# Kernel optimization log

Measured on AMD Instinct MI355X. Metric: run time of the kernel, lower is better.

## Reference

```python
import jax, jax.numpy as jnp
import numpy as np

D_IN = 1024
D_OUT = 1024
N_HEADS = 16
HEAD_DIM = D_OUT // N_HEADS


def setup_inputs() -> dict:
    key = jax.random.key(0)
    ks = jax.random.split(key, 6)
    s = 0.02
    return {
        "x": jax.random.normal(ks[0], (2, 2048, D_IN), dtype=jnp.float32),
        "W_q": jax.random.normal(ks[1], (D_IN, D_OUT), dtype=jnp.float32) * s,
        "W_k": jax.random.normal(ks[2], (D_IN, D_OUT), dtype=jnp.float32) * s,
        "W_v": jax.random.normal(ks[3], (D_IN, D_OUT), dtype=jnp.float32) * s,
        "W_o": jax.random.normal(ks[4], (D_OUT, D_OUT), dtype=jnp.float32) * s,
        "b_o": jax.random.normal(ks[5], (D_OUT,), dtype=jnp.float32) * s,
    }


def reference(x, W_q, W_k, W_v, W_o, b_o):
    B, S, _ = x.shape
    # projections -> [B, H, S, Dh]
    def split_heads(t):
        return t.reshape(B, S, N_HEADS, HEAD_DIM).transpose(0, 2, 1, 3)
    q = split_heads(x @ W_q)
    k = split_heads(x @ W_k)
    v = split_heads(x @ W_v)
    scores = jnp.einsum("bhqd,bhkd->bhqk", q, k)
    causal = jnp.triu(jnp.ones((S, S), dtype=bool), k=1)  # True above diagonal
    scores = jnp.where(causal, -jnp.inf, scores)
    attn = jax.nn.softmax(scores / jnp.sqrt(jnp.float32(HEAD_DIM)), axis=-1)
    ctx = jnp.einsum("bhqk,bhkd->bhqd", attn, v)  # [B,H,S,Dh]
    ctx = ctx.transpose(0, 2, 1, 3).reshape(B, S, D_OUT)
    return ctx @ W_o + b_o
```

## Files before the change

kernel.cpp:

```cpp
#include <hip/hip_runtime.h>
#include <math.h>

typedef unsigned short u16;
typedef unsigned int u32;
typedef short v8s __attribute__((ext_vector_type(8)));
typedef float v4f __attribute__((ext_vector_type(4)));
typedef u16 u16x4v __attribute__((ext_vector_type(4)));
typedef u16 u16x8v __attribute__((ext_vector_type(8)));
typedef u32 u32x2 __attribute__((ext_vector_type(2)));

#define S_LEN 2048
#define D_MODEL 1024
#define DH 64
#define BS_ROWS 4096

#define QSCALE 0.1803368801111204f

#if __has_builtin(__builtin_amdgcn_exp2f)
#define EXP2(x) __builtin_amdgcn_exp2f(x)
#else
#define EXP2(x) __expf(0.6931471805599453f * (x))
#endif

__device__ __forceinline__ u16 f2bf(float f) {
    union { float f; unsigned int u; } c; c.f = f;
    unsigned int u = c.u;
    unsigned int r = (u + 0x7FFFu + ((u >> 16) & 1u)) >> 16;
    return (u16)r;
}
__device__ __forceinline__ u32 pack2bf(float a, float b) {
    u32 ua = __float_as_uint(a) + 0x8000u;
    u32 ub = __float_as_uint(b) + 0x8000u;
    return (ua >> 16) | (ub & 0xFFFF0000u);
}

__device__ __forceinline__ v4f mfma16(v8s a, v8s b, v4f c) {
    return __builtin_amdgcn_mfma_f32_16x16x32_bf16(a, b, c, 0, 0, 0);
}

__device__ __forceinline__ void gl_lds(const u16* g, u16* l) {
    __builtin_amdgcn_global_load_lds(
        (const __attribute__((address_space(1))) void*)g,
        (__attribute__((address_space(3))) void*)l, 16, 0, 0);
}

__global__ __launch_bounds__(256) void prep_kernel(const float* __restrict__ x,
                                                   const float* __restrict__ Wq,
                                                   const float* __restrict__ Wk,
                                                   const float* __restrict__ Wv,
                                                   const float* __restrict__ Wo,
                                                   u16* __restrict__ xb,
                                                   u16* __restrict__ wqkv,
                                                   u16* __restrict__ wo_t) {
    __shared__ u16 tile[64][72];
    int blk = blockIdx.x;
    int t = threadIdx.x;
    if (blk < 4096) {
        int i = blk * 256 + t;
        float4 v = ((const float4*)x)[i];
        u16x4v o;
        o[0] = f2bf(v.x); o[1] = f2bf(v.y); o[2] = f2bf(v.z); o[3] = f2bf(v.w);
        ((u16x4v*)xb)[i] = o;
        return;
    }
    int pb = blk - 4096;
    int z = pb >> 8;
    pb &= 255;
    const float* w = (z == 0) ? Wq : (z == 1) ? Wk : (z == 2) ? Wv : Wo;
    u16* wt = (z < 3) ? (wqkv + (size_t)z * 1024 * 1024) : wo_t;
    int k0 = (pb & 15) * 64, n0 = (pb >> 4) * 64;
    int tr = t >> 4;
    int tc = (t & 15) * 4;
#pragma unroll
    for (int i = 0; i < 4; ++i) {
        int k = tr + 16 * i;
        float4 v = *(const float4*)(w + (size_t)(k0 + k) * 1024 + n0 + tc);
        tile[tc + 0][k] = f2bf(v.x);
        tile[tc + 1][k] = f2bf(v.y);
        tile[tc + 2][k] = f2bf(v.z);
        tile[tc + 3][k] = f2bf(v.w);
    }
    __syncthreads();
#pragma unroll
    for (int i = 0; i < 4; ++i) {
        int n = tr + 16 * i;
        u16x4v o;
        o[0] = tile[n][tc]; o[1] = tile[n][tc + 1];
        o[2] = tile[n][tc + 2]; o[3] = tile[n][tc + 3];
        *(u16x4v*)(wt + (size_t)(n0 + n) * 1024 + k0 + tc) = o;
    }
}

template <int MODE>
__global__ __launch_bounds__(256, 3) void gemm_kernel(
    const u16* __restrict__ A, const u16* __restrict__ Bt,
    const float* __restrict__ bias,
    u16* __restrict__ q_out, u16* __restrict__ k_out, u16* __restrict__ v_out,
    float* __restrict__ out_f32) {
    constexpr int BN = (MODE == 0) ? 128 : 64;
    constexpr int MT = (MODE == 0) ? 4 : 2;
    constexpr int K = 1024;
    __shared__ __align__(16) u16 Smem[128 * 64 + BN * 64];
    u16* As = Smem;
    u16* Bs = Smem + 128 * 64;
    int tid = threadIdx.x;
    int lane = tid & 63;
    int w = tid >> 6;
    int n16 = lane & 15, quad = lane >> 4;
    int lrow = lane >> 3, lchunk = lane & 7;
    int m0 = blockIdx.y * 128, n0 = blockIdx.x * BN;
    int wm_off = (MODE == 0) ? (w >> 1) * 64 : w * 32;
    int wn_off = (MODE == 0) ? (w & 1) * 64 : 0;

    v4f acc[MT][4];
#pragma unroll
    for (int i = 0; i < MT; ++i)
#pragma unroll
        for (int j = 0; j < 4; ++j) acc[i][j] = v4f{0, 0, 0, 0};

    for (int k0 = 0; k0 < K; k0 += 64) {
#pragma unroll
        for (int i = 0; i < 4; ++i) {
            int r = w * 32 + i * 8 + lrow;
            int gc = lchunk ^ (r & 7);
            gl_lds(A + (size_t)(m0 + r) * K + k0 + gc * 8, As + (w * 32 + i * 8) * 64);
        }
        if (MODE == 0) {
#pragma unroll
            for (int i = 0; i < 4; ++i) {
                int r = w * 32 + i * 8 + lrow;
                int gc = lchunk ^ (r & 7);
                gl_lds(Bt + (size_t)(n0 + r) * K + k0 + gc * 8, Bs + (w * 32 + i * 8) * 64);
            }
        } else {
#pragma unroll
            for (int i = 0; i < 2; ++i) {
                int r = w * 16 + i * 8 + lrow;
                int gc = lchunk ^ (r & 7);
                gl_lds(Bt + (size_t)(n0 + r) * K + k0 + gc * 8, Bs + (w * 16 + i * 8) * 64);
            }
        }
        __syncthreads();
#pragma unroll
        for (int kk = 0; kk < 64; kk += 32) {
            v8s af[MT], bf[4];
#pragma unroll
            for (int mt = 0; mt < MT; ++mt) {
                int ra = wm_off + mt * 16 + n16;
                af[mt] = *(const v8s*)(As + ra * 64 + ((((kk >> 3) + quad) ^ (ra & 7)) << 3));
            }
#pragma unroll
            for (int nt = 0; nt < 4; ++nt) {
                int rb = wn_off + nt * 16 + n16;
                bf[nt] = *(const v8s*)(Bs + rb * 64 + ((((kk >> 3) + quad) ^ (rb & 7)) << 3));
            }
#pragma unroll
            for (int mt = 0; mt < MT; ++mt)
#pragma unroll
                for (int nt = 0; nt < 4; ++nt)
                    acc[mt][nt] = mfma16(af[mt], bf[nt], acc[mt][nt]);
        }
        __syncthreads();
    }

    if (MODE == 1) {
#pragma unroll
        for (int mt = 0; mt < MT; ++mt)
#pragma unroll
            for (int nt = 0; nt < 4; ++nt)
#pragma unroll
                for (int r = 0; r < 4; ++r) {
                    int row = m0 + wm_off + mt * 16 + quad * 4 + r;
                    int col = n0 + nt * 16 + n16;
                    out_f32[(size_t)row * 1024 + col] = acc[mt][nt][r] + bias[col];
                }
        return;
    }

    int which = n0 >> 10;
    if (which < 2) {
        u16* dst = which ? k_out : q_out;
        float sc = which ? 1.0f : QSCALE;
#pragma unroll
        for (int mt = 0; mt < 4; ++mt)
#pragma unroll
            for (int nt = 0; nt < 4; ++nt) {
                int colb = n0 + wn_off + nt * 16;
                int rowb = m0 + wm_off + mt * 16 + quad * 4;
                int hb = (colb & 1023) >> 6;
                int d = (colb & 63) + n16;
                int b = rowb >> 11, s = rowb & 2047;
                int bh = b * 16 + hb;
#pragma unroll
                for (int r = 0; r < 4; ++r)
                    dst[((size_t)bh * S_LEN + s + r) * DH + d] = f2bf(acc[mt][nt][r] * sc);
            }
    } else {
        int b = m0 >> 11, s0 = m0 & 2047;
        u16* T = Smem;
#pragma unroll
        for (int p = 0; p < 2; ++p) {
            __syncthreads();
            if ((w & 1) == p) {
#pragma unroll
                for (int mt = 0; mt < 4; ++mt)
#pragma unroll
                    for (int nt = 0; nt < 4; ++nt) {
                        int d = nt * 16 + n16;
                        int sl = (w >> 1) * 64 + mt * 16 + quad * 4;
                        u16x4v pk;
#pragma unroll
                        for (int r = 0; r < 4; ++r) pk[r] = f2bf(acc[mt][nt][r]);
                        *(u16x4v*)(T + d * 136 + sl) = pk;
                    }
            }
            __syncthreads();
            int h = 2 * (blockIdx.x - 16) + p;
            int bh = b * 16 + h;
            int d = tid >> 2;
            int part = tid & 3;
            u16* gp = v_out + ((size_t)bh * DH + d) * S_LEN + s0 + part * 32;
            const u16* tp = T + d * 136 + part * 32;
#pragma unroll
            for (int i = 0; i < 4; ++i)
                *(u16x8v*)(gp + i * 8) = *(const u16x8v*)(tp + i * 8);
        }
    }
}

template <bool DIAG>
__device__ __forceinline__ void attn_step(const u16* __restrict__ ks,
                                          const u16* __restrict__ vs,
                                          u16* __restrict__ pw,
                                          v8s qa0, v8s qa1,
                                          v4f* acc, float& l,
                                          int n16, int quad, int wq) {
    v4f st[4];
#pragma unroll
    for (int nt = 0; nt < 4; ++nt) {
        int rk = nt * 16 + n16;
        const u16* kr = ks + rk * 64;
        v4f t = v4f{0, 0, 0, 0};
        t = mfma16(*(const v8s*)(kr + ((quad ^ (rk & 7)) << 3)), qa0, t);
        t = mfma16(*(const v8s*)(kr + (((4 + quad) ^ (rk & 7)) << 3)), qa1, t);
        st[nt] = t;
    }
    int h = n16 & 7;
    u16* prow = pw + n16 * 64;
#pragma unroll
    for (int nt = 0; nt < 4; ++nt) {
        float e[4];
#pragma unroll
        for (int r = 0; r < 4; ++r) {
            float v = EXP2(st[nt][r]);
            if (DIAG) {
                if (nt * 16 + quad * 4 + r > wq) v = 0.0f;
            }
            e[r] = v;
            l += v;
        }
        u32x2 pk;
        pk[0] = pack2bf(e[0], e[1]);
        pk[1] = pack2bf(e[2], e[3]);
        *(u32x2*)(prow + (((2 * nt + (quad >> 1)) ^ h) << 3) + (quad & 1) * 4) = pk;
    }
    v8s pa0 = *(const v8s*)(prow + ((quad ^ h) << 3));
    v8s pa1 = *(const v8s*)(prow + (((4 + quad) ^ h) << 3));
#pragma unroll
    for (int f = 0; f < 4; ++f) {
        int rv = f * 16 + n16;
        const u16* vr = vs + rv * 64;
        acc[f] = mfma16(pa0, *(const v8s*)(vr + ((quad ^ (rv & 7)) << 3)), acc[f]);
        acc[f] = mfma16(pa1, *(const v8s*)(vr + (((4 + quad) ^ (rv & 7)) << 3)), acc[f]);
    }
}

__global__ __launch_bounds__(256, 4) void attn_kernel(const u16* __restrict__ Qg,
                                                      const u16* __restrict__ Kg,
                                                      const u16* __restrict__ Vtg,
                                                      u16* __restrict__ ctx) {
    __shared__ __align__(16) u16 Ks[2][64 * 64];
    __shared__ __align__(16) u16 Vs[2][64 * 64];
    __shared__ __align__(16) u16 Ps[4][16 * 64];

    int i = blockIdx.x;
    int xcd = i & 7;
    int j = i >> 3;
    int bh = xcd * 4 + (j & 3);
    int idx = j >> 2;
    int i0 = idx & 7, m = idx >> 3;
    int qt = (m == 0) ? (31 - i0) : (m == 1) ? (16 + i0) : (m == 2) ? (15 - i0) : i0;
    int qbase = qt * 64;
    int tid = threadIdx.x;
    int w = tid >> 6;
    int lane = tid & 63;
    int n16 = lane & 15;
    int quad = lane >> 4;
    int lrow = lane >> 3, lchunk = lane & 7;

    const u16* Qb = Qg + (size_t)bh * (S_LEN * DH);
    const u16* Kb = Kg + (size_t)bh * (S_LEN * DH);
    const u16* Vtb = Vtg + (size_t)bh * (S_LEN * DH);
    u16* pw = Ps[w];
    int b = bh >> 4, h = bh & 15;
    int cur = 0;

    auto stage = [&](int kb, int buf) {
#pragma unroll
        for (int i2 = 0; i2 < 2; ++i2) {
            int r = w * 16 + i2 * 8 + lrow;
            int gc = lchunk ^ (r & 7);
            gl_lds(Kb + (size_t)(kb + r) * DH + gc * 8, &Ks[buf][(w * 16 + i2 * 8) * 64]);
            gl_lds(Vtb + (size_t)r * S_LEN + kb + gc * 8, &Vs[buf][(w * 16 + i2 * 8) * 64]);
        }
    };

    int qrow = qbase + w * 16 + n16;
    v8s qa0 = *(const v8s*)(Qb + (size_t)qrow * DH + quad * 8);
    v8s qa1 = *(const v8s*)(Qb + (size_t)qrow * DH + 32 + quad * 8);

    v4f acc[4];
#pragma unroll
    for (int f = 0; f < 4; ++f) acc[f] = v4f{0, 0, 0, 0};
    float l = 0.0f;
    int wq = w * 16 + n16;
    int nkb = qt + 1;

    stage(0, cur);
    for (int it = 0; it < nkb - 1; ++it) {
        __syncthreads();
        stage((it + 1) * 64, cur ^ 1);
        attn_step<false>(Ks[cur], Vs[cur], pw, qa0, qa1, acc, l, n16, quad, wq);
        cur ^= 1;
    }
    __syncthreads();
    attn_step<true>(Ks[cur], Vs[cur], pw, qa0, qa1, acc, l, n16, quad, wq);

    l += __shfl_xor(l, 16);
    l += __shfl_xor(l, 32);
#pragma unroll
    for (int r = 0; r < 4; ++r) {
        float lq = __shfl(l, quad * 4 + r);
        float inv = 1.0f / lq;
        int srow = qbase + w * 16 + quad * 4 + r;
        size_t base = ((size_t)(b * S_LEN + srow)) * D_MODEL + h * DH;
#pragma unroll
        for (int f = 0; f < 4; ++f)
            ctx[base + f * 16 + n16] = f2bf(acc[f][r] * inv);
    }
}

extern "C" void kernel_launch(void* const* d_in, const int* in_sizes, int n_in,
                              void* d_out, int out_size, void* d_ws, size_t ws_size,
                              hipStream_t stream) {
    const float* x  = (const float*)d_in[0];
    const float* Wq = (const float*)d_in[1];
    const float* Wk = (const float*)d_in[2];
    const float* Wv = (const float*)d_in[3];
    const float* Wo = (const float*)d_in[4];
    const float* bo = (const float*)d_in[5];
    float* out = (float*)d_out;

    char* ws = (char*)d_ws;
    u16* x_bf = (u16*)ws;   ws += (size_t)BS_ROWS * D_MODEL * 2;
    u16* wqkv = (u16*)ws;   ws += (size_t)3 * D_MODEL * D_MODEL * 2;
    u16* wo_t = (u16*)ws;   ws += (size_t)D_MODEL * D_MODEL * 2;
    u16* qbuf = (u16*)ws;   ws += (size_t)BS_ROWS * D_MODEL * 2;
    u16* kbuf = (u16*)ws;   ws += (size_t)BS_ROWS * D_MODEL * 2;
    u16* vtbuf = (u16*)ws;  ws += (size_t)BS_ROWS * D_MODEL * 2;
    u16* ctx = (u16*)ws;    ws += (size_t)BS_ROWS * D_MODEL * 2;

    prep_kernel<<<5120, 256, 0, stream>>>(x, Wq, Wk, Wv, Wo, x_bf, wqkv, wo_t);

    gemm_kernel<0><<<dim3(24, 32), 256, 0, stream>>>(x_bf, wqkv, nullptr,
                                                     qbuf, kbuf, vtbuf, nullptr);
    attn_kernel<<<1024, 256, 0, stream>>>(qbuf, kbuf, vtbuf, ctx);
    gemm_kernel<1><<<dim3(16, 32), 256, 0, stream>>>(ctx, wo_t, bo,
                                                     nullptr, nullptr, nullptr, out);
}
```

Before: 165.0 us.

## Process two 64-row query tiles per attention block to reuse staged K/V

```diff
diff --git a/kernel.cpp b/kernel.cpp
--- a/kernel.cpp
+++ b/kernel.cpp
@@ -275,7 +275,7 @@
     }
 }
 
-__global__ __launch_bounds__(256, 4) void attn_kernel(const u16* __restrict__ Qg,
+__global__ __launch_bounds__(256, 2) void attn_kernel(const u16* __restrict__ Qg,
                                                       const u16* __restrict__ Kg,
                                                       const u16* __restrict__ Vtg,
                                                       u16* __restrict__ ctx) {
@@ -283,14 +283,16 @@
     __shared__ __align__(16) u16 Vs[2][64 * 64];
     __shared__ __align__(16) u16 Ps[4][16 * 64];
 
-    int i = blockIdx.x;
-    int xcd = i & 7;
-    int j = i >> 3;
-    int bh = xcd * 4 + (j & 3);
-    int idx = j >> 2;
-    int i0 = idx & 7, m = idx >> 3;
-    int qt = (m == 0) ? (31 - i0) : (m == 1) ? (16 + i0) : (m == 2) ? (15 - i0) : i0;
-    int qbase = qt * 64;
+    int jj = blockIdx.x;
+    int xcd = jj & 7;
+    int jp = jj >> 3;
+    int t = jp & 3, u = jp >> 2;
+    int bh = xcd * 4 + t;
+    int us = (u + 4) & 15;
+    int b0 = (u < 8) ? u : 23 - u;
+    int b0s = (us < 8) ? us : 23 - us;
+    int qt = (t == 0) ? b0 : (t == 1) ? 15 - b0 : (t == 2) ? b0s : 15 - b0s;
+    int qbase = qt * 128;
     int tid = threadIdx.x;
     int w = tid >> 6;
     int lane = tid & 63;
@@ -310,43 +312,58 @@
         for (int i2 = 0; i2 < 2; ++i2) {
             int r = w * 16 + i2 * 8 + lrow;
             int gc = lchunk ^ (r & 7);
-            gl_lds(Kb + (size_t)(kb + r) * DH + gc * 8, &Ks[buf][(w * 16 + i2 * 8) * 64]);
-            gl_lds(Vtb + (size_t)r * S_LEN + kb + gc * 8, &Vs[buf][(w * 16 + i2 * 8) * 64]);
+            gl_lds(Kb + (size_t)(kb * 64 + r) * DH + gc * 8, &Ks[buf][(w * 16 + i2 * 8) * 64]);
+            gl_lds(Vtb + (size_t)r * S_LEN + kb * 64 + gc * 8, &Vs[buf][(w * 16 + i2 * 8) * 64]);
         }
     };
 
-    int qrow = qbase + w * 16 + n16;
-    v8s qa0 = *(const v8s*)(Qb + (size_t)qrow * DH + quad * 8);
-    v8s qa1 = *(const v8s*)(Qb + (size_t)qrow * DH + 32 + quad * 8);
-
-    v4f acc[4];
-#pragma unroll
-    for (int f = 0; f < 4; ++f) acc[f] = v4f{0, 0, 0, 0};
-    float l = 0.0f;
+    v8s qa0[2], qa1[2];
+#pragma unroll
+    for (int g = 0; g < 2; ++g) {
+        int qrow = qbase + g * 64 + w * 16 + n16;
+        qa0[g] = *(const v8s*)(Qb + (size_t)qrow * DH + quad * 8);
+        qa1[g] = *(const v8s*)(Qb + (size_t)qrow * DH + 32 + quad * 8);
+    }
+
+    v4f acc[2][4];
+#pragma unroll
+    for (int g = 0; g < 2; ++g)
+#pragma unroll
+        for (int f = 0; f < 4; ++f) acc[g][f] = v4f{0, 0, 0, 0};
+    float l0 = 0.0f, l1 = 0.0f;
     int wq = w * 16 + n16;
-    int nkb = qt + 1;
-
-    stage(0, cur);
-    for (int it = 0; it < nkb - 1; ++it) {
+
+    stage(0, 0);
+    for (int it = 0; it < 2 * qt; ++it) {
         __syncthreads();
-        stage((it + 1) * 64, cur ^ 1);
-        attn_step<false>(Ks[cur], Vs[cur], pw, qa0, qa1, acc, l, n16, quad, wq);
+        stage(it + 1, cur ^ 1);
+        attn_step<false>(Ks[cur], Vs[cur], pw, qa0[0], qa1[0], acc[0], l0, n16, quad, wq);
+        attn_step<false>(Ks[cur], Vs[cur], pw, qa0[1], qa1[1], acc[1], l1, n16, quad, wq);
         cur ^= 1;
     }
     __syncthreads();
-    attn_step<true>(Ks[cur], Vs[cur], pw, qa0, qa1, acc, l, n16, quad, wq);
-
-    l += __shfl_xor(l, 16);
-    l += __shfl_xor(l, 32);
-#pragma unroll
-    for (int r = 0; r < 4; ++r) {
-        float lq = __shfl(l, quad * 4 + r);
-        float inv = 1.0f / lq;
-        int srow = qbase + w * 16 + quad * 4 + r;
-        size_t base = ((size_t)(b * S_LEN + srow)) * D_MODEL + h * DH;
-#pragma unroll
-        for (int f = 0; f < 4; ++f)
-            ctx[base + f * 16 + n16] = f2bf(acc[f][r] * inv);
+    stage(2 * qt + 1, cur ^ 1);
+    attn_step<true >(Ks[cur], Vs[cur], pw, qa0[0], qa1[0], acc[0], l0, n16, quad, wq);
+    attn_step<false>(Ks[cur], Vs[cur], pw, qa0[1], qa1[1], acc[1], l1, n16, quad, wq);
+    cur ^= 1;
+    __syncthreads();
+    attn_step<true >(Ks[cur], Vs[cur], pw, qa0[1], qa1[1], acc[1], l1, n16, quad, wq);
+
+#pragma unroll
+    for (int g = 0; g < 2; ++g) {
+        float l = g ? l1 : l0;
+        l += __shfl_xor(l, 16);
+        l += __shfl_xor(l, 32);
+#pragma unroll
+        for (int r = 0; r < 4; ++r) {
+            float lq = __shfl(l, quad * 4 + r);
+            float inv = 1.0f / lq;
+            int srow = qbase + g * 64 + w * 16 + quad * 4 + r;
+            size_t base = ((size_t)(b * S_LEN + srow)) * D_MODEL + h * DH;
+#pragma unroll
+            for (int f = 0; f < 4; ++f)
+                ctx[base + f * 16 + n16] = f2bf(acc[g][f][r] * inv);
+        }
     }
 }
 
@@ -374,7 +391,7 @@
 
     gemm_kernel<0><<<dim3(24, 32), 256, 0, stream>>>(x_bf, wqkv, nullptr,
                                                      qbuf, kbuf, vtbuf, nullptr);
-    attn_kernel<<<1024, 256, 0, stream>>>(qbuf, kbuf, vtbuf, ctx);
+    attn_kernel<<<512, 256, 0, stream>>>(qbuf, kbuf, vtbuf, ctx);
     gemm_kernel<1><<<dim3(16, 32), 256, 0, stream>>>(ctx, wo_t, bo,
                                                      nullptr, nullptr, nullptr, out);
 }
```

After: 175.9 us. 6.6% more time.
